# Optimization experiments

Hardware: AMD Instinct MI355X
Metric: run time of the kernel (lower is better)

Reference implementation:

```python
import jax, jax.numpy as jnp
import numpy as np

N_Q = 8        # qubits
DENC = 3       # encoding entangling layers
DVAR = 3       # variational entangling layers
SEQ = 64
BATCH = 256
D_FEAT = N_Q * (DENC + 2)   # 40, per-token feature dim
D_W = N_Q * (DVAR + 2)      # 40, per-position weight dim


def _rx(t):
    c = jnp.cos(t / 2).astype(jnp.complex64)
    s = (-1j * jnp.sin(t / 2)).astype(jnp.complex64)
    return jnp.stack([jnp.stack([c, s]), jnp.stack([s, c])])


def _ry(t):
    c = jnp.cos(t / 2)
    s = jnp.sin(t / 2)
    return jnp.stack([jnp.stack([c, -s]), jnp.stack([s, c])]).astype(jnp.complex64)


def _apply1(state, U, wire):
    # state: (2,)*N_Q complex; apply 2x2 gate on `wire`
    s = jnp.tensordot(U, state, axes=([1], [wire]))
    return jnp.moveaxis(s, 0, wire)


def _cnot(state, c, t):
    s0 = jnp.take(state, 0, axis=c)
    s1 = jnpp_flip = jnp.take(state, 1, axis=c)
    t2 = t - 1 if t > c else t
    s1 = jnp.flip(s1, axis=t2)  # X on target when control=1
    return jnp.stack([s0, s1], axis=c)


def _circuit(x, w, sign):
    # x: [D_FEAT] encoding angles, w: [D_W] variational angles
    state = jnp.zeros((2,) * N_Q, jnp.complex64).at[(0,) * N_Q].set(1.0)
    idx = 0
    for j in range(N_Q):
        state = _apply1(state, _rx(x[idx]), j)
        state = _apply1(state, _ry(x[idx + 1]), j)
        idx += 2
    for _ in range(DENC):
        for j in range(N_Q):
            state = _cnot(state, j, (j + 1) % N_Q)
        for j in range(N_Q):
            state = _apply1(state, _ry(x[idx]), j)
            idx += 1
    idx = 0
    for j in range(N_Q):
        state = _apply1(state, _rx(w[idx]), j)
        state = _apply1(state, _ry(w[idx + 1]), j)
        idx += 2
    for _ in range(DVAR):
        for j in range(N_Q):
            state = _cnot(state, j, (j + 1) % N_Q)
        for j in range(N_Q):
            state = _apply1(state, _ry(w[idx]), j)
            idx += 1
    probs = (jnp.abs(state) ** 2).astype(jnp.float32)
    return jnp.sum(probs * sign)


# observable sign tables
_Z0 = jnp.array([1.0, -1.0], jnp.float32).reshape((2,) + (1,) * (N_Q - 1))
_ZALL = jnp.array([1.0, -1.0], jnp.float32)
for _ in range(N_Q - 1):
    _ZALL = _ZALL[..., None] * jnp.array([1.0, -1.0], jnp.float32)


def _batched(sign):
    f = lambda xx, ww: _circuit(xx, ww, sign)
    f = jax.vmap(f, in_axes=(0, 0))      # over seq positions (per-position weights)
    return jax.vmap(f, in_axes=(0, None))  # over batch


_qk = _batched(_Z0)
_v = _batched(_ZALL)  # random_op fixed deterministically to Z x Z x ... x Z


def setup_inputs() -> dict:
    key = jax.random.key(0)
    k1, k2, k3, k4 = jax.random.split(key, 4)
    scale = np.float32(np.pi / 4)
    x = jax.random.normal(k1, (BATCH, SEQ, D_FEAT), jnp.float32)
    pQ = scale * (2 * jax.random.normal(k2, (SEQ, D_W), jnp.float32) - 1)
    pK = scale * (2 * jax.random.normal(k3, (SEQ, D_W), jnp.float32) - 1)
    pV = scale * (2 * jax.random.normal(k4, (SEQ, D_W), jnp.float32) - 1)
    return {"x": x, "params_Q": pQ, "params_K": pK, "params_V": pV}


def reference(x, params_Q, params_K, params_V):
    # Per-token quantum circuit sims -> scalar Q, K, V expectations
    Q = _qk(x, params_Q)   # [B, S]
    K = _qk(x, params_K)   # [B, S]
    V = _v(x, params_V)    # [B, S]  (original returns d identical copies of this)
    # Gaussian-kernel attention: alpha[b,i,m] = exp(-(Q_i - K_m)^2)
    alpha = jnp.exp(-(Q[:, :, None] - K[:, None, :]) ** 2)   # [B, S, S]
    w = alpha / jnp.sum(alpha, axis=-1, keepdims=True)
    att = jnp.einsum('bim,bm->bi', w, V)                     # [B, S]
    return x + att[:, :, None]  # broadcast over d (V copies are identical)
```

## Files before the change

kernel.cpp:

```cpp
#include <hip/hip_runtime.h>

#define SEQd 64
#define BATCHd 256
#define DF 40

typedef float f2 __attribute__((ext_vector_type(2)));
typedef __fp16 h2v __attribute__((ext_vector_type(2)));


template<int LM>
__device__ __forceinline__ float xch1(float v) {
  if constexpr (LM == 0) {
    return v;
  } else if constexpr (LM == 1 || LM == 2 || LM == 3 || LM == 7) {
    constexpr int ctrl = (LM == 1) ? 0xB1 : (LM == 2) ? 0x4E : (LM == 3) ? 0x1B
                       : 0x141;
    return __int_as_float(__builtin_amdgcn_mov_dpp(__float_as_int(v), ctrl, 0xF, 0xF, true));
  } else {
    return __int_as_float(__builtin_amdgcn_ds_swizzle(__float_as_int(v), (LM << 10) | 0x1F));
  }
}

template<int LM>
__device__ __forceinline__ f2 xch2(f2 v) {
  if constexpr (LM == 0) return v;
  f2 r; r.x = xch1<LM>(v.x); r.y = xch1<LM>(v.y); return r;
}

__device__ __forceinline__ f2 ff(f2 x, f2 y, f2 z) { return __builtin_elementwise_fma(x, y, z); }
__device__ __forceinline__ f2 cmul(f2 a, f2 b) {
  f2 r; r.x = a.x * b.x - a.y * b.y; r.y = a.x * b.y + a.y * b.x; return r;
}
__device__ __forceinline__ f2 uget(float4 f, bool bit) {
  f2 r; r.x = bit ? f.z : f.x; r.y = bit ? -f.w : f.y; return r;
}

template<int M, int SM>
__device__ __forceinline__ void ry32(f2* a, f2 cs, int lam) {
  constexpr int LM = M & 7, RM = M >> 3, SL = SM & 7, SR = SM >> 3;
  float t0;
  if constexpr (SL != 0) t0 = (__popc(lam & SL) & 1) ? cs.y : -cs.y;
  else                   t0 = -cs.y;
  const f2 cv = {cs.x, cs.x};
  const f2 tp = {t0, t0}, tn = {-t0, -t0};
#pragma unroll
  for (int k = 0; k < 32; ++k) {
    const int kp = k ^ RM;
    if (kp < k) continue;
    if (kp == k) {
      const f2 b = xch2<LM>(a[k]);
      a[k] = ff(b, (__builtin_popcount(k & SR) & 1) ? tn : tp, a[k] * cv);
    } else {
      const f2 b0 = xch2<LM>(a[kp]);
      const f2 b1 = xch2<LM>(a[k]);
      const f2 t_k  = (__builtin_popcount(k  & SR) & 1) ? tn : tp;
      const f2 t_kp = (__builtin_popcount(kp & SR) & 1) ? tn : tp;
      a[k]  = ff(b0, t_k,  a[k]  * cv);
      a[kp] = ff(b1, t_kp, a[kp] * cv);
    }
  }
}

template<int M, int SM>
__device__ __forceinline__ void su2_32(f2* a, float4 q, int lam) {
  constexpr int LM = M & 7, RM = M >> 3, SL = SM & 7, SR = SM >> 3;
  float sb, sc;
  if constexpr (SL != 0) {
    const bool p = (__popc(lam & SL) & 1) != 0;
    sb = p ? -q.y : q.y; sc = p ? -q.z : q.z;
  } else { sb = q.y; sc = q.z; }
  const f2 vqa = {q.x, q.x};
  const f2 vqw = {q.w, -q.w};
  const f2 vfc0 = {-sc, -sc}, vfb0 = {-sb, sb};
  const f2 vfc1 = { sc,  sc}, vfb1 = { sb, -sb};
#pragma unroll
  for (int k = 0; k < 32; ++k) {
    const int kp = k ^ RM;
    if (kp < k) continue;
    if (kp == k) {
      const f2 B = xch2<LM>(a[k]);
      const bool pk = (__builtin_popcount(k & SR) & 1) != 0;
      const f2 A = a[k];
      f2 r = A * vqa;
      r = ff(B, pk ? vfc1 : vfc0, r);
      r = ff(A.yx, pk ? vfb1 : vfb0, r);
      r = ff(B.yx, vqw, r);
      a[k] = r;
    } else {
      const f2 B0 = xch2<LM>(a[kp]);
      const f2 B1 = xch2<LM>(a[k]);
      const bool pk0 = (__builtin_popcount(k  & SR) & 1) != 0;
      const bool pk1 = (__builtin_popcount(kp & SR) & 1) != 0;
      const f2 A0 = a[k], A1 = a[kp];
      f2 r0 = A0 * vqa;
      r0 = ff(B0, pk0 ? vfc1 : vfc0, r0);
      r0 = ff(A0.yx, pk0 ? vfb1 : vfb0, r0);
      r0 = ff(B0.yx, vqw, r0);
      a[k] = r0;
      f2 r1 = A1 * vqa;
      r1 = ff(B1, pk1 ? vfc1 : vfc0, r1);
      r1 = ff(A1.yx, pk1 ? vfb1 : vfb0, r1);
      r1 = ff(B1.yx, vqw, r1);
      a[kp] = r1;
    }
  }
}

__device__ __forceinline__ void layers32(f2* a, const f2* __restrict__ L, int lam) {
  ry32<0xC0,0x7F>(a, L[0],  lam);
  ry32<0x60,0xC0>(a, L[1],  lam);
  ry32<0x30,0xE0>(a, L[2],  lam);
  ry32<0x18,0xF0>(a, L[3],  lam);
  ry32<0x0C,0xF8>(a, L[4],  lam);
  ry32<0x06,0xFC>(a, L[5],  lam);
  ry32<0x03,0xFE>(a, L[6],  lam);
  ry32<0xC1,0xFF>(a, L[7],  lam);
  ry32<0xA0,0xD5>(a, L[8],  lam);
  ry32<0x50,0xBF>(a, L[9],  lam);
  ry32<0x28,0x5F>(a, L[10], lam);
  ry32<0x14,0xAF>(a, L[11], lam);
  ry32<0x0A,0x57>(a, L[12], lam);
  ry32<0x05,0xAB>(a, L[13], lam);
  ry32<0xC2,0x55>(a, L[14], lam);
  ry32<0x61,0xAA>(a, L[15], lam);
  ry32<0xF0,0x4C>(a, L[16], lam);
  ry32<0x78,0x6A>(a, L[17], lam);
  ry32<0x3C,0x35>(a, L[18], lam);
  ry32<0x1E,0x9A>(a, L[19], lam);
  ry32<0x0F,0xCD>(a, L[20], lam);
  ry32<0xC7,0x66>(a, L[21], lam);
  ry32<0xA3,0x33>(a, L[22], lam);
  ry32<0x91,0x99>(a, L[23], lam);
}

__device__ __forceinline__ void initial32(f2* a, const float4* __restrict__ F, int lam) {
  su2_32<0x80,0x80>(a, F[0], lam);
  su2_32<0x40,0x40>(a, F[1], lam);
  su2_32<0x20,0x20>(a, F[2], lam);
  su2_32<0x10,0x10>(a, F[3], lam);
  su2_32<0x08,0x08>(a, F[4], lam);
  su2_32<0x04,0x04>(a, F[5], lam);
  su2_32<0x02,0x02>(a, F[6], lam);
  su2_32<0x01,0x01>(a, F[7], lam);
}

__device__ __forceinline__ void pinit32(f2* a, const float4* __restrict__ F, int lam) {
  f2 c = {1.f, 0.f};
#pragma unroll
  for (int i = 0; i < 3; ++i)
    c = cmul(c, uget(F[7 - i], ((lam >> i) & 1) != 0));
  f2 wlo[4], whi[8];
#pragma unroll
  for (int t = 0; t < 4; ++t)
    wlo[t] = cmul(uget(F[4], (t & 1) != 0), uget(F[3], ((t >> 1) & 1) != 0));
#pragma unroll
  for (int t = 0; t < 8; ++t)
    whi[t] = cmul(cmul(uget(F[2], (t & 1) != 0), uget(F[1], ((t >> 1) & 1) != 0)),
                  uget(F[0], ((t >> 2) & 1) != 0));
#pragma unroll
  for (int k = 0; k < 32; ++k)
    a[k] = cmul(cmul(c, wlo[k & 3]), whi[k >> 2]);
}

__device__ __forceinline__ uint32_t packh(f2 v) {
  h2v h = __builtin_amdgcn_cvt_pkrtz(v.x, v.y);
  return __builtin_bit_cast(uint32_t, h);
}
__device__ __forceinline__ f2 unpackh(uint32_t u) {
  h2v h = __builtin_bit_cast(h2v, u);
  f2 r; r.x = (float)h[0]; r.y = (float)h[1]; return r;
}

__device__ __forceinline__ void snap_write32(const f2* a, uint32_t* sn, int lam) {
  int tgt = 0;
  if (lam & 1) tgt ^= 0x2B;
  if (lam & 2) tgt ^= 0x56;
  if (lam & 4) tgt ^= 0xAC;
#pragma unroll
  for (int k = 0; k < 32; ++k) {
    const int rck = ((k & 1) ? 0xD9 : 0) ^ ((k & 2) ? 0x33 : 0) ^ ((k & 4) ? 0x66 : 0)
                  ^ ((k & 8) ? 0xCC : 0) ^ ((k & 16) ? 0x19 : 0);
    const int qq = tgt ^ rck;
    sn[((qq & 7) << 5) | (qq >> 3)] = packh(a[k]);
  }
}

__device__ __forceinline__ void snap_read32(f2* a, const uint32_t* sn, int lam) {
  const uint4* p = (const uint4*)(sn + lam * 32);
#pragma unroll
  for (int t = 0; t < 8; ++t) {
    const uint4 w = p[t];
    a[4*t+0] = unpackh(w.x); a[4*t+1] = unpackh(w.y);
    a[4*t+2] = unpackh(w.z); a[4*t+3] = unpackh(w.w);
  }
}

template<int SM>
__device__ __forceinline__ float expect32(const f2* a, int lam) {
  constexpr int SL = SM & 7, SR = SM >> 3;
  float s0 = 0.f, s1 = 0.f;
#pragma unroll
  for (int k = 0; k < 32; ++k) {
    const float p = a[k].x * a[k].x + a[k].y * a[k].y;
    if ((__builtin_popcount(k & SR) & 1) != 0) s1 += p; else s0 += p;
  }
  const float d = s0 - s1;
  float v;
  if constexpr (SL != 0) v = (__popc(lam & SL) & 1) ? -d : d;
  else                   v = d;
  v += xch1<1>(v); v += xch1<2>(v); v += xch1<4>(v);
  return v;
}

__global__ __launch_bounds__(256) void prep_var(
    const float* __restrict__ pQ, const float* __restrict__ pK,
    const float* __restrict__ pV, float* __restrict__ vtab)
{
  const int t = blockIdx.x * 256 + threadIdx.x;
  if (t >= SEQd * 3 * 32) return;
  const int slot = t & 31;
  const int sh = t >> 5;
  const int h = sh % 3, sp = sh / 3;
  const float* w = ((h == 0) ? pQ : (h == 1) ? pK : pV) + sp * DF;
  float* o = vtab + sh * 80;
  if (slot < 8) {
    float cx, sx, cy, sy;
    __sincosf(w[2 * slot]     * 0.5f, &sx, &cx);
    __sincosf(w[2 * slot + 1] * 0.5f, &sy, &cy);
    ((float4*)o)[slot] = make_float4(cy * cx, sy * sx, sy * cx, cy * sx);
  } else {
    float sn, cn;
    __sincosf(w[16 + (slot - 8)] * 0.5f, &sn, &cn);
    ((float2*)(o + 32))[slot - 8] = make_float2(cn, sn);
  }
}

__global__ __launch_bounds__(256) void qsal_circuits(
    const float* __restrict__ x, const float* __restrict__ vtab,
    float* __restrict__ Qo, float* __restrict__ Ko, float* __restrict__ Vo)
{
  __shared__ __align__(16) float etab[8][84];
  __shared__ __align__(16) uint32_t snap[8][264];
  const int tid = threadIdx.x;
  const int wid = tid >> 6, lane = tid & 63;
  const int ci = lane >> 3, lam = lane & 7;
  const int s = blockIdx.x & 63;
  const int bbase = (blockIdx.x >> 6) << 3;

  for (int t = tid; t < 320; t += 256) {
    const int cc = t / 40, idx = t - cc * 40;
    const float ang = x[((size_t)(bbase + cc) * 64 + s) * 40 + idx];
    float sn, cn; __sincosf(ang * 0.5f, &sn, &cn);
    if (idx < 16) {
      const int wire = idx >> 1, isy = idx & 1;
      etab[cc][wire * 4 + isy * 2 + 0] = cn;
      etab[cc][wire * 4 + isy * 2 + 1] = sn;
    } else {
      etab[cc][32 + (idx - 16) * 2 + 0] = cn;
      etab[cc][32 + (idx - 16) * 2 + 1] = sn;
    }
  }
  __syncthreads();
  if (tid < 64) {
    const int cc = tid >> 3, wire = tid & 7;
    float4* qt = (float4*)etab[cc];
    const float4 f = qt[wire];
    qt[wire] = make_float4(f.z * f.x, f.w * f.y, f.w * f.x, f.z * f.y);
  }
  __syncthreads();

  if (wid == 0) {
    f2 a[32];
    pinit32(a, (const float4*)etab[ci], lam);
    layers32(a, (const f2*)(etab[ci] + 32), lam);
    snap_write32(a, snap[ci], lam);
  }
  __syncthreads();

  if (wid >= 1) {
    const int h = wid - 1;
    const float* th = vtab + s * 240 + 80 * h;
    f2 v[32];
    snap_read32(v, snap[ci], lam);
    initial32(v, (const float4*)th, lam);
    layers32(v, (const f2*)(th + 32), lam);
    const float e = (h == 2) ? expect32<0x88>(v, lam) : expect32<0x4C>(v, lam);
    if (lam == 0) {
      float* op = (h == 0) ? Qo : (h == 1) ? Ko : Vo;
      op[(bbase + ci) * 64 + s] = e;
    }
  }
}

__global__ __launch_bounds__(256) void qsal_attn(
    const float* __restrict__ x,
    const float* __restrict__ Qv,
    const float* __restrict__ Kv,
    const float* __restrict__ Vv,
    float* __restrict__ out)
{
  const int tid  = threadIdx.x;
  const int wid  = tid >> 6;
  const int lane = tid & 63;
  const int bi   = blockIdx.x * 4 + wid;
  const int b    = bi >> 6;

  const float q = Qv[bi];
  const float k = Kv[b * 64 + lane];
  const float v = Vv[b * 64 + lane];
  const float d = q - k;
  float e  = __expf(-d * d);
  float ev = e * v;
#pragma unroll
  for (int m = 1; m < 64; m <<= 1) {
    e  += __shfl_xor(e,  m, 64);
    ev += __shfl_xor(ev, m, 64);
  }
  const float att = ev / e;

  const size_t row = (size_t)bi * DF;
  if (lane < DF) out[row + lane] = x[row + lane] + att;
}

extern "C" void kernel_launch(void* const* d_in, const int* in_sizes, int n_in,
                              void* d_out, int out_size, void* d_ws, size_t ws_size,
                              hipStream_t stream) {
  const float* x  = (const float*)d_in[0];
  const float* pQ = (const float*)d_in[1];
  const float* pK = (const float*)d_in[2];
  const float* pV = (const float*)d_in[3];
  float* out = (float*)d_out;

  float* Qv   = (float*)d_ws;
  float* Kv   = Qv + BATCHd * SEQd;
  float* Vv   = Kv + BATCHd * SEQd;
  float* vtab = Vv + BATCHd * SEQd;

  prep_var<<<dim3(24), dim3(256), 0, stream>>>(pQ, pK, pV, vtab);
  qsal_circuits<<<dim3(2048), dim3(256), 0, stream>>>(x, vtab, Qv, Kv, Vv);
  qsal_attn<<<dim3(BATCHd * SEQd / 4), dim3(256), 0, stream>>>(x, Qv, Kv, Vv, out);
}
```

Measured before the change: 90.17 us.

## Make every wave run all four circuit phases on its own 8 batches

Before, wave 0 of each block ran the shared encoding circuit while the other three waves sat idle, and then those three ran the Q, K and V circuits. Now each block handles 32 batches, and every wave runs the encoding phase and then the Q, K and V phases in sequence for its own 8 batches. The per-position variational table is staged in shared memory, the snapshot row stride is padded to 36 words to reduce bank conflicts, and the grid shrinks to 512 blocks with a launch-bounds occupancy hint. This removes the serial phase where three quarters of each block idled, at the cost of a larger shared-memory footprint and fewer, longer blocks.

```diff
diff --git a/kernel.cpp b/kernel.cpp
--- a/kernel.cpp
+++ b/kernel.cpp
@@ -181,12 +181,12 @@
     const int rck = ((k & 1) ? 0xD9 : 0) ^ ((k & 2) ? 0x33 : 0) ^ ((k & 4) ? 0x66 : 0)
                   ^ ((k & 8) ? 0xCC : 0) ^ ((k & 16) ? 0x19 : 0);
     const int qq = tgt ^ rck;
-    sn[((qq & 7) << 5) | (qq >> 3)] = packh(a[k]);
+    sn[(qq & 7) * 36 + (qq >> 3)] = packh(a[k]);
   }
 }
 
 __device__ __forceinline__ void snap_read32(f2* a, const uint32_t* sn, int lam) {
-  const uint4* p = (const uint4*)(sn + lam * 32);
+  const uint4* p = (const uint4*)(sn + lam * 36);
 #pragma unroll
   for (int t = 0; t < 8; ++t) {
     const uint4 w = p[t];
@@ -235,19 +235,21 @@
   }
 }
 
-__global__ __launch_bounds__(256) void qsal_circuits(
+__global__ __launch_bounds__(256, 3) void qsal_circuits(
     const float* __restrict__ x, const float* __restrict__ vtab,
     float* __restrict__ Qo, float* __restrict__ Ko, float* __restrict__ Vo)
 {
-  __shared__ __align__(16) float etab[8][84];
-  __shared__ __align__(16) uint32_t snap[8][264];
+  __shared__ __align__(16) float etab[32][84];
+  __shared__ __align__(16) uint32_t snap[32][296];
+  __shared__ __align__(16) float vtabs[240];
   const int tid = threadIdx.x;
   const int wid = tid >> 6, lane = tid & 63;
-  const int ci = lane >> 3, lam = lane & 7;
+  const int lam = lane & 7;
+  const int cig = (wid << 3) | (lane >> 3);
   const int s = blockIdx.x & 63;
-  const int bbase = (blockIdx.x >> 6) << 3;
-
-  for (int t = tid; t < 320; t += 256) {
+  const int bbase = (blockIdx.x >> 6) << 5;
+
+  for (int t = tid; t < 1280; t += 256) {
     const int cc = t / 40, idx = t - cc * 40;
     const float ang = x[((size_t)(bbase + cc) * 64 + s) * 40 + idx];
     float sn, cn; __sincosf(ang * 0.5f, &sn, &cn);
@@ -260,8 +262,9 @@
       etab[cc][32 + (idx - 16) * 2 + 1] = sn;
     }
   }
+  if (tid < 60) ((float4*)vtabs)[tid] = ((const float4*)(vtab + s * 240))[tid];
   __syncthreads();
-  if (tid < 64) {
+  {
     const int cc = tid >> 3, wire = tid & 7;
     float4* qt = (float4*)etab[cc];
     const float4 f = qt[wire];
@@ -269,26 +272,30 @@
   }
   __syncthreads();
 
-  if (wid == 0) {
-    f2 a[32];
-    pinit32(a, (const float4*)etab[ci], lam);
-    layers32(a, (const f2*)(etab[ci] + 32), lam);
-    snap_write32(a, snap[ci], lam);
-  }
-  __syncthreads();
-
-  if (wid >= 1) {
-    const int h = wid - 1;
-    const float* th = vtab + s * 240 + 80 * h;
-    f2 v[32];
-    snap_read32(v, snap[ci], lam);
-    initial32(v, (const float4*)th, lam);
-    layers32(v, (const f2*)(th + 32), lam);
-    const float e = (h == 2) ? expect32<0x88>(v, lam) : expect32<0x4C>(v, lam);
-    if (lam == 0) {
-      float* op = (h == 0) ? Qo : (h == 1) ? Ko : Vo;
-      op[(bbase + ci) * 64 + s] = e;
-    }
+  f2 st[32];
+#pragma unroll 1
+  for (int ph = 0; ph < 4; ++ph) {
+    const f2* L;
+    if (ph == 0) {
+      pinit32(st, (const float4*)etab[cig], lam);
+      L = (const f2*)(etab[cig] + 32);
+    } else {
+      snap_read32(st, snap[cig], lam);
+      const float* th = vtabs + (ph - 1) * 80;
+      initial32(st, (const float4*)th, lam);
+      L = (const f2*)(th + 32);
+    }
+    layers32(st, L, lam);
+    if (ph == 0) {
+      snap_write32(st, snap[cig], lam);
+    } else {
+      const float e = (ph == 3) ? expect32<0x88>(st, lam) : expect32<0x4C>(st, lam);
+      if (lam == 0) {
+        float* op = (ph == 1) ? Qo : (ph == 2) ? Ko : Vo;
+        op[(bbase + cig) * 64 + s] = e;
+      }
+    }
+    __syncthreads();
   }
 }
 
@@ -337,6 +344,6 @@
   float* vtab = Vv + BATCHd * SEQd;
 
   prep_var<<<dim3(24), dim3(256), 0, stream>>>(pQ, pK, pV, vtab);
-  qsal_circuits<<<dim3(2048), dim3(256), 0, stream>>>(x, vtab, Qv, Kv, Vv);
+  qsal_circuits<<<dim3(512), dim3(256), 0, stream>>>(x, vtab, Qv, Kv, Vv);
   qsal_attn<<<dim3(BATCHd * SEQd / 4), dim3(256), 0, stream>>>(x, Qv, Kv, Vv, out);
 }
```

Result: faster. 76.90 us (-14.7%).
